# Kernel tuning notes

Hardware: AMD Instinct MI355X
Metric: run time of the kernel (lower is better)

## Reference

```python
import jax, jax.numpy as jnp
import numpy as np

H, D, G = 8, 64, 64          # num_heads, head_dim, num_slices
HID = H * D                  # 512
EPS = 1e-5
N = 100000


def setup_inputs() -> dict:
    key = jax.random.key(0)
    ks = jax.random.split(key, 16)
    s = 0.02  # init scale
    return {
        "x": jax.random.normal(ks[0], (N, HID), dtype=jnp.float32),
        # x_proj / fx_proj: Linear(HID -> HID) with bias, eqx stores W as (out, in)
        "Wx": jax.random.normal(ks[1], (HID, HID), dtype=jnp.float32) * s,
        "bx": jax.random.normal(ks[2], (HID,), dtype=jnp.float32) * s,
        "Wfx": jax.random.normal(ks[3], (HID, HID), dtype=jnp.float32) * s,
        "bfx": jax.random.normal(ks[4], (HID,), dtype=jnp.float32) * s,
        # slice_proj: Linear(D -> G) with bias
        "Ws": jax.random.normal(ks[5], (G, D), dtype=jnp.float32) * s,
        "bs": jax.random.normal(ks[6], (G,), dtype=jnp.float32) * s,
        # learned temperature, init 0.5, shape (H,1,1)
        "temperature": jnp.ones((H, 1, 1), dtype=jnp.float32) * 0.5,
        # slice MultiheadAttention (num_heads=1, size D): q/k/v/out proj, no biases (eqx defaults)
        "Wq": jax.random.normal(ks[7], (D, D), dtype=jnp.float32) * s,
        "Wk": jax.random.normal(ks[8], (D, D), dtype=jnp.float32) * s,
        "Wv": jax.random.normal(ks[9], (D, D), dtype=jnp.float32) * s,
        "Wo": jax.random.normal(ks[10], (D, D), dtype=jnp.float32) * s,
        # out_proj: Linear(HID -> HID) with bias
        "Wout": jax.random.normal(ks[11], (HID, HID), dtype=jnp.float32) * s,
        "bout": jax.random.normal(ks[12], (HID,), dtype=jnp.float32) * s,
    }


def reference(x, Wx, bx, Wfx, bfx, Ws, bs, temperature, Wq, Wk, Wv, Wo, Wout, bout):
    n = x.shape[0]
    # token projections, split into heads: (H, N, D)
    x_mid = (x @ Wx.T + bx).reshape(n, H, D).transpose(1, 0, 2)
    fx_mid = (x @ Wfx.T + bfx).reshape(n, H, D).transpose(1, 0, 2)

    # slice weights: proj -> temperature-scaled softmax over G  (H, N, G)
    logits = jnp.einsum('hnd,gd->hng', x_mid, Ws) + bs
    w = jax.nn.softmax(logits * temperature, axis=-1)

    # weighted pooling to slice tokens (H, G, D)
    norm = w.sum(axis=1)                                   # (H, G)
    tokens = jnp.einsum('hnd,hng->hgd', fx_mid, w) / (norm[..., None] + EPS)

    # small single-head attention over the G slice tokens, vmapped over H
    q = jnp.einsum('hgd,od->hgo', tokens, Wq)
    k = jnp.einsum('hgd,od->hgo', tokens, Wk)
    v = jnp.einsum('hgd,od->hgo', tokens, Wv)
    attn = jax.nn.softmax(jnp.einsum('hgd,hkd->hgk', q, k) / jnp.sqrt(jnp.float32(D)), axis=-1)
    out_tok = jnp.einsum('hgk,hkd->hgd', attn, v)
    out_tok = jnp.einsum('hgd,od->hgo', out_tok, Wo)

    # deslice: weighted unpooling back to tokens, merge heads, output projection
    out = jnp.einsum('hgd,hng->hnd', out_tok, w)           # (H, N, D)
    out = out.transpose(1, 0, 2).reshape(n, HID)
    return out @ Wout.T + bout
```

## Files before the change

kernel.cpp:

```cpp
#include <hip/hip_runtime.h>
#include <hip/hip_bf16.h>

#define HID 512
#define NH  8
#define DD  64
#define GG  64
#define EPSF 1e-5f

typedef __attribute__((ext_vector_type(8))) short short8;
typedef __attribute__((ext_vector_type(4))) short short4v;
typedef __attribute__((ext_vector_type(4))) float floatx4;

__device__ __forceinline__ short f2bf(float f) {
    union { float f; unsigned u; } v; v.f = f;
    unsigned r = v.u + 0x7fffu + ((v.u >> 16) & 1u);
    return (short)(r >> 16);
}
__device__ __forceinline__ float bf2f(short s) {
    union { unsigned u; float f; } v;
    v.u = ((unsigned)(unsigned short)s) << 16;
    return v.f;
}

#define GLOAD_LDS16(g, l) __builtin_amdgcn_global_load_lds( \
    (const __attribute__((address_space(1))) unsigned int*)(g), \
    (__attribute__((address_space(3))) unsigned int*)(l), 16, 0, 0)

__global__ __launch_bounds__(256)
void cast_kernel(const float* __restrict__ x, short* __restrict__ xb, int n8) {
    int i = blockIdx.x * 256 + threadIdx.x;
    if (i >= n8) return;
    const float4* p = (const float4*)(x + (size_t)i * 8);
    float4 a = p[0], b = p[1];
    short8 v;
    v[0] = f2bf(a.x); v[1] = f2bf(a.y); v[2] = f2bf(a.z); v[3] = f2bf(a.w);
    v[4] = f2bf(b.x); v[5] = f2bf(b.y); v[6] = f2bf(b.z); v[7] = f2bf(b.w);
    *(short8*)(xb + (size_t)i * 8) = v;
}

__global__ void fold1_kernel(const float* __restrict__ Wx, const float* __restrict__ bx,
                             const float* __restrict__ Wfx, const float* __restrict__ bfx,
                             const float* __restrict__ Ws, const float* __restrict__ bs,
                             const float* __restrict__ temp,
                             short* __restrict__ Wcat, float* __restrict__ bias_cat) {
    int idx = blockIdx.x * 256 + threadIdx.x;
    int row = idx >> 9;
    int k = idx & 511;
    float val;
    if (row < 512) {
        val = Wfx[row * 512 + k];
        if (k == 0) bias_cat[row] = bfx[row];
    } else {
        int hg = row - 512;
        int h = hg >> 6, g = hg & 63;
        float t = temp[h];
        float s = 0.f;
        #pragma unroll 8
        for (int d = 0; d < 64; ++d) s += Ws[g * 64 + d] * Wx[(h * 64 + d) * 512 + k];
        val = s * t;
        if (k == 0) {
            float b = 0.f;
            for (int d = 0; d < 64; ++d) b += Ws[g * 64 + d] * bx[h * 64 + d];
            bias_cat[row] = (b + bs[g]) * t;
        }
    }
    Wcat[idx] = f2bf(val);
}

template <bool OUT_F32, bool FUSE_SM>
__global__ __launch_bounds__(256, 4)
void gemm_bt(const short* __restrict__ A, int lda,
             const short* __restrict__ B,
             const float* __restrict__ bias,
             void* __restrict__ Cp, int ldc,
             int M, int K, int clog2, int Rtiles) {
    __shared__ short As[128 * 32];
    __shared__ short Bs[128 * 32];

    const int id = blockIdx.x;
    const int xcd = id & 7;
    const int s = id >> 3;
    const int cblk = s & ((1 << clog2) - 1);
    const int slice = (Rtiles + 7) >> 3;
    const int rt = xcd * slice + (s >> clog2);
    if (rt >= Rtiles) return;

    const int tid = threadIdx.x;
    const int wid = tid >> 6, lane = tid & 63;
    const int col0 = cblk * 128;
    const int row0 = rt * 128;
    const int wm = (wid >> 1) * 64, wn = (wid & 1) * 64;
    const int lr = lane & 15, lq = lane >> 4;

    int st_row[2], st_kc[2];
    #pragma unroll
    for (int it = 0; it < 2; ++it) {
        int c = tid + it * 256;
        st_row[it] = c >> 2;
        st_kc[it] = (c & 3) ^ ((st_row[it] >> 1) & 3);
    }
    const int fx_ = lq ^ ((lr >> 1) & 3);

    floatx4 acc[4][4];
    #pragma unroll
    for (int i = 0; i < 4; ++i)
        #pragma unroll
        for (int j = 0; j < 4; ++j) acc[i][j] = (floatx4)(0.f);

    const short* Abase = A + (size_t)row0 * lda;
    const short* Bbase = B + (size_t)col0 * lda;

    for (int k0 = 0; k0 < K; k0 += 32) {
        #pragma unroll
        for (int it = 0; it < 2; ++it) {
            short* ldsA = As + (wid * 64 + it * 256) * 8;
            short* ldsB = Bs + (wid * 64 + it * 256) * 8;
            GLOAD_LDS16(Abase + (size_t)st_row[it] * lda + k0 + st_kc[it] * 8, ldsA);
            GLOAD_LDS16(Bbase + (size_t)st_row[it] * lda + k0 + st_kc[it] * 8, ldsB);
        }
        __syncthreads();

        short8 af[4], bfr[4];
        #pragma unroll
        for (int i = 0; i < 4; ++i) af[i]  = *(const short8*)&As[(wm + i * 16 + lr) * 32 + fx_ * 8];
        #pragma unroll
        for (int j = 0; j < 4; ++j) bfr[j] = *(const short8*)&Bs[(wn + j * 16 + lr) * 32 + fx_ * 8];
        #pragma unroll
        for (int i = 0; i < 4; ++i)
            #pragma unroll
            for (int j = 0; j < 4; ++j)
                acc[i][j] = __builtin_amdgcn_mfma_f32_16x16x32_bf16(af[i], bfr[j], acc[i][j], 0, 0, 0);
        __syncthreads();
    }

    const bool do_sm = FUSE_SM && (col0 >= 512);
    float bcol[4];
    #pragma unroll
    for (int j = 0; j < 4; ++j) bcol[j] = bias[col0 + wn + j * 16 + lr];

    #pragma unroll
    for (int i = 0; i < 4; ++i) {
        #pragma unroll
        for (int r = 0; r < 4; ++r) {
            int grow = row0 + wm + i * 16 + lq * 4 + r;
            float v[4];
            #pragma unroll
            for (int j = 0; j < 4; ++j) v[j] = acc[i][j][r] + bcol[j];
            if (do_sm) {
                float m = fmaxf(fmaxf(v[0], v[1]), fmaxf(v[2], v[3]));
                #pragma unroll
                for (int off = 1; off < 16; off <<= 1) m = fmaxf(m, __shfl_xor(m, off));
                float sum = 0.f;
                #pragma unroll
                for (int j = 0; j < 4; ++j) { v[j] = __expf(v[j] - m); sum += v[j]; }
                #pragma unroll
                for (int off = 1; off < 16; off <<= 1) sum += __shfl_xor(sum, off);
                float inv = 1.f / sum;
                #pragma unroll
                for (int j = 0; j < 4; ++j) v[j] *= inv;
            }
            if (grow < M) {
                #pragma unroll
                for (int j = 0; j < 4; ++j) {
                    int gcol = col0 + wn + j * 16 + lr;
                    if constexpr (OUT_F32) ((float*)Cp)[(size_t)grow * ldc + gcol] = v[j];
                    else                   ((short*)Cp)[(size_t)grow * ldc + gcol] = f2bf(v[j]);
                }
            }
        }
    }
}

__global__ __launch_bounds__(256)
void pool_kernel(const short* __restrict__ mid, float* __restrict__ tok_raw,
                 float* __restrict__ norm, int N, int chunk) {
    int h = blockIdx.y;
    int n0 = blockIdx.x * chunk;
    int n1 = min(n0 + chunk, N);
    int tid = threadIdx.x;
    int gi = tid >> 4, di = tid & 15;
    __shared__ short ws_[16][64];
    __shared__ short fs_[16][64];
    float c[4][4] = {};
    float nrm[4] = {};
    for (int nb = n0; nb < n1; nb += 16) {
        int nrows = min(16, n1 - nb);
        {
            int r = tid >> 4;
            int seg = tid & 15;
            int n = nb + r;
            short8 v = (short8)(0);
            if (n < n1) {
                if (seg < 8) v = *(const short8*)(mid + (size_t)n * 1024 + 512 + h * 64 + seg * 8);
                else         v = *(const short8*)(mid + (size_t)n * 1024 + h * 64 + (seg - 8) * 8);
            }
            if (seg < 8) *(short8*)&ws_[r][seg * 8] = v;
            else         *(short8*)&fs_[r][(seg - 8) * 8] = v;
        }
        __syncthreads();
        for (int r = 0; r < nrows; ++r) {
            short4v a = *(const short4v*)&ws_[r][gi * 4];
            short4v b = *(const short4v*)&fs_[r][di * 4];
            float wv[4], fv[4];
            wv[0] = bf2f(a.x); wv[1] = bf2f(a.y); wv[2] = bf2f(a.z); wv[3] = bf2f(a.w);
            fv[0] = bf2f(b.x); fv[1] = bf2f(b.y); fv[2] = bf2f(b.z); fv[3] = bf2f(b.w);
            #pragma unroll
            for (int i = 0; i < 4; ++i)
                #pragma unroll
                for (int j = 0; j < 4; ++j) c[i][j] += wv[i] * fv[j];
            if (di == 0) {
                #pragma unroll
                for (int i = 0; i < 4; ++i) nrm[i] += wv[i];
            }
        }
        __syncthreads();
    }
    #pragma unroll
    for (int i = 0; i < 4; ++i)
        #pragma unroll
        for (int j = 0; j < 4; ++j)
            atomicAdd(&tok_raw[(h * 64 + gi * 4 + i) * 64 + di * 4 + j], c[i][j]);
    if (di == 0) {
        #pragma unroll
        for (int i = 0; i < 4; ++i) atomicAdd(&norm[h * 64 + gi * 4 + i], nrm[i]);
    }
}

__global__ __launch_bounds__(256)
void attn_kernel(const float* __restrict__ tok_raw, const float* __restrict__ norm,
                 const float* __restrict__ Wq, const float* __restrict__ Wk,
                 const float* __restrict__ Wv, const float* __restrict__ Wo,
                 float* __restrict__ out_tok) {
    const int h = blockIdx.x;
    const int tid = threadIdx.x;
    const int g = tid & 63, part = tid >> 6;
    const int o0 = part * 16;

    __shared__ float tk[64][65];
    __shared__ float qq[64][65];
    __shared__ float kk[64][65];
    __shared__ float vv[64][65];
    __shared__ float pp[64][65];
    __shared__ float od[64][65];

    const float inv = 1.f / (norm[h * 64 + g] + EPSF);
    #pragma unroll
    for (int dd = 0; dd < 16; ++dd) {
        int d = o0 + dd;
        tk[g][d] = tok_raw[(size_t)(h * 64 + g) * 64 + d] * inv;
    }
    __syncthreads();

    float t[64];
    #pragma unroll
    for (int d = 0; d < 64; ++d) t[d] = tk[g][d];
    #pragma unroll
    for (int oo = 0; oo < 16; ++oo) {
        int o = o0 + oo;
        float sq = 0.f, sk = 0.f, sv = 0.f;
        #pragma unroll
        for (int d = 0; d < 64; ++d) {
            float td = t[d];
            sq += td * Wq[o * 64 + d];
            sk += td * Wk[o * 64 + d];
            sv += td * Wv[o * 64 + d];
        }
        qq[g][o] = sq; kk[g][o] = sk; vv[g][o] = sv;
    }
    __syncthreads();

    float q[64];
    #pragma unroll
    for (int o = 0; o < 64; ++o) q[o] = qq[g][o];
    #pragma unroll
    for (int jj = 0; jj < 16; ++jj) {
        int j = o0 + jj;
        float s = 0.f;
        #pragma unroll
        for (int o = 0; o < 64; ++o) s += q[o] * kk[j][o];
        pp[g][j] = s * 0.125f;
    }
    __syncthreads();

    float sr[64];
    float mx = -1e30f;
    #pragma unroll
    for (int j = 0; j < 64; ++j) { sr[j] = pp[g][j]; mx = fmaxf(mx, sr[j]); }
    float sum = 0.f;
    #pragma unroll
    for (int j = 0; j < 64; ++j) { sr[j] = __expf(sr[j] - mx); sum += sr[j]; }
    const float isum = 1.f / sum;

    #pragma unroll
    for (int dd = 0; dd < 16; ++dd) {
        int d = o0 + dd;
        float a = 0.f;
        #pragma unroll
        for (int j = 0; j < 64; ++j) a += sr[j] * vv[j][d];
        od[g][d] = a * isum;
    }
    __syncthreads();

    float ot[64];
    #pragma unroll
    for (int d = 0; d < 64; ++d) ot[d] = od[g][d];
    #pragma unroll
    for (int oo = 0; oo < 16; ++oo) {
        int o = o0 + oo;
        float a = 0.f;
        #pragma unroll
        for (int d = 0; d < 64; ++d) a += ot[d] * Wo[o * 64 + d];
        out_tok[(size_t)(h * 64 + g) * 64 + o] = a;
    }
}

__global__ void fold2_kernel(const float* __restrict__ out_tok,
                             const float* __restrict__ Wout, short* __restrict__ Vbf) {
    int idx = blockIdx.x * 256 + threadIdx.x;
    int o = idx >> 9, hg = idx & 511;
    int h = hg >> 6;
    const float* ot = out_tok + (size_t)hg * 64;
    const float* wo = Wout + (size_t)o * 512 + h * 64;
    float s = 0.f;
    #pragma unroll 8
    for (int d = 0; d < 64; ++d) s += ot[d] * wo[d];
    Vbf[idx] = f2bf(s);
}

extern "C" void kernel_launch(void* const* d_in, const int* in_sizes, int n_in,
                              void* d_out, int out_size, void* d_ws, size_t ws_size,
                              hipStream_t stream) {
    const float* x    = (const float*)d_in[0];
    const float* Wx   = (const float*)d_in[1];
    const float* bx   = (const float*)d_in[2];
    const float* Wfx  = (const float*)d_in[3];
    const float* bfx  = (const float*)d_in[4];
    const float* Ws   = (const float*)d_in[5];
    const float* bs   = (const float*)d_in[6];
    const float* temp = (const float*)d_in[7];
    const float* Wq   = (const float*)d_in[8];
    const float* Wk   = (const float*)d_in[9];
    const float* Wv   = (const float*)d_in[10];
    const float* Wo   = (const float*)d_in[11];
    const float* Wout = (const float*)d_in[12];
    const float* bout = (const float*)d_in[13];

    const int N = in_sizes[0] / HID;

    char* p = (char*)d_ws;
    short* mid = (short*)p;           p += (size_t)N * 1024 * 2;
    short* Wcat = (short*)p;          p += (size_t)1024 * 512 * 2;
    float* bias_cat = (float*)p;      p += 1024 * 4;
    float* tok_raw = (float*)p;       p += (size_t)NH * GG * DD * 4;
    float* norm_ = (float*)p;         p += (size_t)NH * GG * 4;
    float* out_tok = (float*)p;       p += (size_t)NH * GG * DD * 4;
    short* Vbf = (short*)p;           p += (size_t)512 * 512 * 2;
    short* x_bf = (short*)d_out;

    cast_kernel<<<(N * 512 / 8 + 255) / 256, 256, 0, stream>>>(x, x_bf, N * 512 / 8);
    fold1_kernel<<<2048, 256, 0, stream>>>(Wx, bx, Wfx, bfx, Ws, bs, temp, Wcat, bias_cat);

    const int R = (N + 127) / 128;
    const int slice = (R + 7) / 8;

    gemm_bt<false, true><<<8 * slice * 8, 256, 0, stream>>>(
        x_bf, HID, Wcat, bias_cat, (void*)mid, 1024, N, 512, 3, R);

    hipMemsetAsync(tok_raw, 0, (size_t)(NH * GG * DD + NH * GG) * 4, stream);

    int chunk = (N + 95) / 96;
    dim3 g2(96, 8);
    pool_kernel<<<g2, 256, 0, stream>>>(mid, tok_raw, norm_, N, chunk);

    attn_kernel<<<8, 256, 0, stream>>>(tok_raw, norm_, Wq, Wk, Wv, Wo, out_tok);

    fold2_kernel<<<1024, 256, 0, stream>>>(out_tok, Wout, Vbf);

    gemm_bt<true, false><<<8 * slice * 4, 256, 0, stream>>>(
        mid + 512, 1024, Vbf, bout, d_out, HID, N, 512, 2, R);
}
```

Baseline: 886.0 us.

## Rewrite slice pooling as bf16 MFMA matmul with ones-vector norm accumulation

Replaces the scalar FMA outer-product pooling kernel with a version built on 16x16x32 bf16 MFMA instructions. Each wave accumulates a 32x32 tile of the G×D slice-token sum and gets the per-slice weight norm from an MFMA against a ones vector. Tiles are staged through padded, swizzled LDS. The grid now uses a fixed 544-row chunk, giving more blocks than the old 96-way split. The trade-off is that the loop only handles whole 32-row steps, so row counts that are not multiples of 32 would silently drop tail rows.

```diff
diff --git a/kernel.cpp b/kernel.cpp
--- a/kernel.cpp
+++ b/kernel.cpp
@@ -172,57 +172,100 @@
 }
 
 __global__ __launch_bounds__(256)
-void pool_kernel(const short* __restrict__ mid, float* __restrict__ tok_raw,
-                 float* __restrict__ norm, int N, int chunk) {
-    int h = blockIdx.y;
-    int n0 = blockIdx.x * chunk;
-    int n1 = min(n0 + chunk, N);
-    int tid = threadIdx.x;
-    int gi = tid >> 4, di = tid & 15;
-    __shared__ short ws_[16][64];
-    __shared__ short fs_[16][64];
-    float c[4][4] = {};
-    float nrm[4] = {};
-    for (int nb = n0; nb < n1; nb += 16) {
-        int nrows = min(16, n1 - nb);
-        {
-            int r = tid >> 4;
-            int seg = tid & 15;
-            int n = nb + r;
-            short8 v = (short8)(0);
-            if (n < n1) {
-                if (seg < 8) v = *(const short8*)(mid + (size_t)n * 1024 + 512 + h * 64 + seg * 8);
-                else         v = *(const short8*)(mid + (size_t)n * 1024 + h * 64 + (seg - 8) * 8);
+void pool_mfma(const short* __restrict__ mid, float* __restrict__ tok_raw,
+               float* __restrict__ norm, int N, int chunk) {
+    const int h = blockIdx.y;
+    const int n0 = blockIdx.x * chunk;
+    if (n0 >= N) return;
+    const int ksteps = (min(chunk, N - n0)) >> 5;
+
+    const int tid = threadIdx.x;
+    const int wid = tid >> 6, lane = tid & 63;
+    const int lr = lane & 15, lq = lane >> 4;
+    const int wg = (wid >> 1) * 32, wd = (wid & 1) * 32;
+
+    __shared__ short wt[32 * 72];
+    __shared__ short ft[32 * 72];
+
+    const int sn = tid >> 3;
+    const int sc0 = (tid & 7) * 8;
+    const int scr = (sc0 + 16 * ((sn >> 3) & 3)) & 63;
+    const int st_off = sn * 72 + scr;
+
+    const int ra = ((wg + lr) + 16 * lq) & 63;
+    const int rb = ((wd + lr) + 16 * lq) & 63;
+
+    const short* wbase = mid + (size_t)n0 * 1024 + 512 + h * 64;
+    const short* fbase = mid + (size_t)n0 * 1024 + h * 64;
+
+    floatx4 acc[2][2];
+    #pragma unroll
+    for (int i = 0; i < 2; ++i)
+        #pragma unroll
+        for (int j = 0; j < 2; ++j) acc[i][j] = (floatx4)(0.f);
+    floatx4 accn[2];
+    accn[0] = (floatx4)(0.f); accn[1] = (floatx4)(0.f);
+
+    short8 ones;
+    #pragma unroll
+    for (int j = 0; j < 8; ++j) ones[j] = (short)0x3F80;
+
+    for (int ks = 0; ks < ksteps; ++ks) {
+        const size_t roff = (size_t)(ks * 32 + sn) * 1024;
+        short8 wv = *(const short8*)(wbase + roff + sc0);
+        short8 fv = *(const short8*)(fbase + roff + sc0);
+        __syncthreads();
+        *(short8*)&wt[st_off] = wv;
+        *(short8*)&ft[st_off] = fv;
+        __syncthreads();
+
+        short8 af[2], bf_[2];
+        #pragma unroll
+        for (int i = 0; i < 2; ++i) {
+            short tmpv[8];
+            #pragma unroll
+            for (int j = 0; j < 8; ++j)
+                tmpv[j] = wt[(lq * 8 + j) * 72 + ((ra + i * 16) & 63)];
+            af[i] = *(const short8*)tmpv;
+        }
+        #pragma unroll
+        for (int j2 = 0; j2 < 2; ++j2) {
+            short tmpv[8];
+            #pragma unroll
+            for (int j = 0; j < 8; ++j)
+                tmpv[j] = ft[(lq * 8 + j) * 72 + ((rb + j2 * 16) & 63)];
+            bf_[j2] = *(const short8*)tmpv;
+        }
+        #pragma unroll
+        for (int i = 0; i < 2; ++i)
+            #pragma unroll
+            for (int j = 0; j < 2; ++j)
+                acc[i][j] = __builtin_amdgcn_mfma_f32_16x16x32_bf16(af[i], bf_[j], acc[i][j], 0, 0, 0);
+        if (wd == 0) {
+            #pragma unroll
+            for (int i = 0; i < 2; ++i)
+                accn[i] = __builtin_amdgcn_mfma_f32_16x16x32_bf16(af[i], ones, accn[i], 0, 0, 0);
+        }
+    }
+
+    #pragma unroll
+    for (int i = 0; i < 2; ++i) {
+        #pragma unroll
+        for (int r = 0; r < 4; ++r) {
+            int g = wg + i * 16 + lq * 4 + r;
+            #pragma unroll
+            for (int j = 0; j < 2; ++j) {
+                int d = wd + j * 16 + lr;
+                atomicAdd(&tok_raw[(h * 64 + g) * 64 + d], acc[i][j][r]);
             }
-            if (seg < 8) *(short8*)&ws_[r][seg * 8] = v;
-            else         *(short8*)&fs_[r][(seg - 8) * 8] = v;
-        }
-        __syncthreads();
-        for (int r = 0; r < nrows; ++r) {
-            short4v a = *(const short4v*)&ws_[r][gi * 4];
-            short4v b = *(const short4v*)&fs_[r][di * 4];
-            float wv[4], fv[4];
-            wv[0] = bf2f(a.x); wv[1] = bf2f(a.y); wv[2] = bf2f(a.z); wv[3] = bf2f(a.w);
-            fv[0] = bf2f(b.x); fv[1] = bf2f(b.y); fv[2] = bf2f(b.z); fv[3] = bf2f(b.w);
-            #pragma unroll
-            for (int i = 0; i < 4; ++i)
-                #pragma unroll
-                for (int j = 0; j < 4; ++j) c[i][j] += wv[i] * fv[j];
-            if (di == 0) {
-                #pragma unroll
-                for (int i = 0; i < 4; ++i) nrm[i] += wv[i];
-            }
-        }
-        __syncthreads();
-    }
-    #pragma unroll
-    for (int i = 0; i < 4; ++i)
-        #pragma unroll
-        for (int j = 0; j < 4; ++j)
-            atomicAdd(&tok_raw[(h * 64 + gi * 4 + i) * 64 + di * 4 + j], c[i][j]);
-    if (di == 0) {
-        #pragma unroll
-        for (int i = 0; i < 4; ++i) atomicAdd(&norm[h * 64 + gi * 4 + i], nrm[i]);
+        }
+    }
+    if (wd == 0 && lr == 0) {
+        #pragma unroll
+        for (int i = 0; i < 2; ++i)
+            #pragma unroll
+            for (int r = 0; r < 4; ++r)
+                atomicAdd(&norm[h * 64 + wg + i * 16 + lq * 4 + r], accn[i][r]);
     }
 }
 
@@ -368,9 +411,9 @@
 
     hipMemsetAsync(tok_raw, 0, (size_t)(NH * GG * DD + NH * GG) * 4, stream);
 
-    int chunk = (N + 95) / 96;
-    dim3 g2(96, 8);
-    pool_kernel<<<g2, 256, 0, stream>>>(mid, tok_raw, norm_, N, chunk);
+    const int chunk = 544;
+    dim3 g2((N + chunk - 1) / chunk, 8);
+    pool_mfma<<<g2, 256, 0, stream>>>(mid, tok_raw, norm_, N, chunk);
 
     attn_kernel<<<8, 256, 0, stream>>>(tok_raw, norm_, Wq, Wk, Wv, Wo, out_tok);
 
```

After: 779.8 us. 12.0% less time.
